# Kernel optimization log

Hardware: AMD Instinct MI355X
Metric: run time of the kernel (lower is better)

The kernel has to match this reference:

```python
import jax, jax.numpy as jnp
import numpy as np

B, C, D = 16, 512, 256
K = 16        # spatio_topk
RD = 128      # rec_dim
H = 8         # num_heads
FFN = 1024    # temporal_ffn
TEMP = 0.5    # temperature


def setup_inputs() -> dict:
    key = jax.random.key(0)
    ks = jax.random.split(key, 8)
    s = lambda k, shape: (jax.random.normal(k, shape, jnp.float32) * 0.02)
    return dict(
        x=jax.random.normal(ks[0], (B, C, D), jnp.float32),
        wq_rec=s(ks[1], (RD, D)),
        wk_rec=s(ks[2], (RD, D)),
        in_proj_w=s(ks[3], (3 * D, D)),
        in_proj_b=jnp.zeros((3 * D,), jnp.float32),
        out_w=s(ks[4], (D, D)),
        out_b=jnp.zeros((D,), jnp.float32),
        ln1_g=jnp.ones((D,), jnp.float32),
        ln1_b=jnp.zeros((D,), jnp.float32),
        mlp_w1=s(ks[5], (FFN, D)),
        mlp_b1=jnp.zeros((FFN,), jnp.float32),
        mlp_w2=s(ks[6], (D, FFN)),
        mlp_b2=jnp.zeros((D,), jnp.float32),
        ln2_g=jnp.ones((D,), jnp.float32),
        ln2_b=jnp.zeros((D,), jnp.float32),
    )


def _ln(x, g, b, eps=1e-5):
    m = x.mean(-1, keepdims=True)
    v = ((x - m) ** 2).mean(-1, keepdims=True)
    return (x - m) * jax.lax.rsqrt(v + eps) * g + b


def reference(x, wq_rec, wk_rec, in_proj_w, in_proj_b, out_w, out_b,
              ln1_g, ln1_b, mlp_w1, mlp_b1, mlp_w2, mlp_b2, ln2_g, ln2_b):
    b, c, d = x.shape
    # --- ST_Rec_Module (training branch: straight-through top-k routing) ---
    xq = x @ wq_rec.T                                   # (B,C,RD)
    xk = x @ wk_rec.T
    logits = jnp.einsum('bqd,bkd->bqk', xq, xk) / TEMP  # (B,C,C)
    idx = jax.lax.top_k(logits, K)[1]                   # (B,C,K)
    z_hard = jax.nn.one_hot(idx, c, dtype=x.dtype)      # (B,C,K,C)
    # cumulative mask of previously-selected channels (exclusive cumsum)
    prev = jnp.cumsum(z_hard, axis=2)
    prev = jnp.concatenate([jnp.zeros_like(prev[:, :, :1]), prev[:, :, :-1]], axis=2)
    mask = prev > 0
    zs = jnp.where(mask, -1e30, logits[:, :, None, :] / TEMP)  # logits/temp twice, as in source
    z_soft = jax.nn.softmax(zs, axis=-1)
    z = z_hard + z_soft - jax.lax.stop_gradient(z_soft)        # straight-through
    rec_x = jnp.einsum('bqkc,bcd->bqkd', z, x)                 # (B,C,K,D)

    # --- ST_Channel_Module: per-channel cross-attention, query length 1 ---
    hd = d // H
    wq, wk, wv = in_proj_w[:d], in_proj_w[d:2 * d], in_proj_w[2 * d:]
    bq, bk, bv = in_proj_b[:d], in_proj_b[d:2 * d], in_proj_b[2 * d:]
    q = (x @ wq.T + bq).reshape(b, c, H, hd)                   # (B,C,H,hd)
    k = (rec_x @ wk.T + bk).reshape(b, c, K, H, hd)
    v = (rec_x @ wv.T + bv).reshape(b, c, K, H, hd)
    scores = jnp.einsum('bchd,bckhd->bchk', q, k) / np.float32(np.sqrt(hd))
    attn = jax.nn.softmax(scores, axis=-1)
    ctx = jnp.einsum('bchk,bckhd->bchd', attn, v).reshape(b, c, d)
    attn_out = ctx @ out_w.T + out_b
    x1 = _ln(attn_out + x, ln1_g, ln1_b)

    # --- ST_Temporal_Module (Identity projections, gelu FFN + LN) ---
    h = jax.nn.gelu(x1 @ mlp_w1.T + mlp_b1, approximate=False)
    h = h @ mlp_w2.T + mlp_b2
    x2 = _ln(h + x1, ln2_g, ln2_b)
    return x2
```

## Files before the change

### kernel.cpp

```cpp
#include <hip/hip_runtime.h>
#include <hip/hip_bf16.h>
#include <math.h>

#define B_   16
#define C_   512
#define D_   256
#define K_   16
#define RD_  128
#define H_   8
#define HD_  32
#define FFN_ 1024
#define M_   (B_ * C_)

typedef __attribute__((ext_vector_type(8))) short bf16x8;
typedef __attribute__((ext_vector_type(4))) float f32x4;

typedef __attribute__((address_space(1))) const int ga_int;
typedef __attribute__((address_space(3))) int ls_int;

static __device__ __forceinline__ short f2bf(float v) {
    __hip_bfloat16 h = __float2bfloat16(v);
    return *(short*)&h;
}
static __device__ __forceinline__ float bf2f(short s) {
    __hip_bfloat16 h = *(__hip_bfloat16*)&s;
    return __bfloat162float(h);
}
static __device__ __forceinline__ float4 ld4bf(const short* p) {
    uint2 u = *(const uint2*)p;
    float4 r;
    r.x = __uint_as_float((u.x & 0xffffu) << 16);
    r.y = __uint_as_float(u.x & 0xffff0000u);
    r.z = __uint_as_float((u.y & 0xffffu) << 16);
    r.w = __uint_as_float(u.y & 0xffff0000u);
    return r;
}

#define N8_X    (M_ * D_ / 8)
#define N8_INW  (768 * D_ / 8)
#define N8_OUTW (D_ * D_ / 8)
#define N8_W1   (FFN_ * D_ / 8)
#define N8_W2   (D_ * FFN_ / 8)
#define N8_WQ   (RD_ * D_ / 8)
#define N8_ALL  (N8_X + N8_INW + N8_OUTW + N8_W1 + N8_W2 + 2 * N8_WQ)

__global__ __launch_bounds__(256) void convert_all_kernel(
    const float* __restrict__ x, const float* __restrict__ inw,
    const float* __restrict__ outw, const float* __restrict__ w1,
    const float* __restrict__ w2, const float* __restrict__ wq,
    const float* __restrict__ wk,
    short* __restrict__ xbf, short* __restrict__ xlo,
    short* __restrict__ inwbf, short* __restrict__ outwbf,
    short* __restrict__ w1bf, short* __restrict__ w2bf,
    short* __restrict__ wqh, short* __restrict__ wql,
    short* __restrict__ wkh, short* __restrict__ wkl)
{
    int i = blockIdx.x * 256 + threadIdx.x;
    if (i >= N8_ALL) return;

    const float* s; short* dh; short* dl = nullptr; int off;
    if      (i < N8_X)                    { s = x;    dh = xbf;    dl = xlo; off = i; }
    else if (i < N8_X + N8_INW)           { s = inw;  dh = inwbf;  off = i - N8_X; }
    else if (i < N8_X + N8_INW + N8_OUTW) { s = outw; dh = outwbf; off = i - N8_X - N8_INW; }
    else if (i < N8_X + N8_INW + N8_OUTW + N8_W1)
                                          { s = w1;   dh = w1bf;   off = i - N8_X - N8_INW - N8_OUTW; }
    else if (i < N8_X + N8_INW + N8_OUTW + N8_W1 + N8_W2)
                                          { s = w2;   dh = w2bf;   off = i - N8_X - N8_INW - N8_OUTW - N8_W1; }
    else if (i < N8_X + N8_INW + N8_OUTW + N8_W1 + N8_W2 + N8_WQ)
                                          { s = wq;   dh = wqh; dl = wql; off = i - N8_X - N8_INW - N8_OUTW - N8_W1 - N8_W2; }
    else                                  { s = wk;   dh = wkh; dl = wkl; off = i - N8_X - N8_INW - N8_OUTW - N8_W1 - N8_W2 - N8_WQ; }

    const float4* sp = (const float4*)s + (size_t)off * 2;
    float4 v0 = sp[0], v1 = sp[1];
    float f[8] = {v0.x, v0.y, v0.z, v0.w, v1.x, v1.y, v1.z, v1.w};
    short rh[8], rl[8];
    #pragma unroll
    for (int j = 0; j < 8; ++j) {
        rh[j] = f2bf(f[j]);
        rl[j] = f2bf(f[j] - bf2f(rh[j]));
    }
    *(bf16x8*)(dh + (size_t)off * 8) = *(bf16x8*)rh;
    if (dl) *(bf16x8*)(dl + (size_t)off * 8) = *(bf16x8*)rl;
}

template<int BM, int BN, int OUT_BF16, int ACT>
__global__ __launch_bounds__(256) void gemm_mfma(
    const short* __restrict__ A, const short* __restrict__ W,
    const float* __restrict__ bias, void* __restrict__ Cout,
    int M, int N, int Kd)
{
    __shared__ short As[2][BM * 32];
    __shared__ short Bs[2][BN * 32];
    const int tid  = threadIdx.x;
    const int wave = tid >> 6;
    const int lane = tid & 63;
    const int bm = blockIdx.y * BM;
    const int bn = blockIdx.x * BN;
    constexpr int MI = BM / 32;
    constexpr int NJ = BN / 32;
    const int wr = (wave >> 1) * (BM / 2);
    const int wc = (wave & 1) * (BN / 2);

    const int fr = lane & 15;
    const int fk = (lane >> 4) * 8;
    const int r0 = tid >> 2, ch = (tid & 3) * 8;

    f32x4 acc[MI][NJ];
    #pragma unroll
    for (int i = 0; i < MI; ++i)
        #pragma unroll
        for (int j = 0; j < NJ; ++j)
            acc[i][j] = (f32x4){0.f, 0.f, 0.f, 0.f};

    auto stage = [&](int buf, int k0) {
        #pragma unroll
        for (int i = 0; i < BM / 64; ++i)
            __builtin_amdgcn_global_load_lds(
                (ga_int*)&A[(size_t)(bm + r0 + i * 64) * Kd + k0 + ch],
                (ls_int*)&As[buf][(tid + i * 256) * 8], 16, 0, 0);
        #pragma unroll
        for (int j = 0; j < BN / 64; ++j)
            __builtin_amdgcn_global_load_lds(
                (ga_int*)&W[(size_t)(bn + r0 + j * 64) * Kd + k0 + ch],
                (ls_int*)&Bs[buf][(tid + j * 256) * 8], 16, 0, 0);
    };

    stage(0, 0);
    int cur = 0;

    for (int k0 = 0; k0 < Kd; k0 += 32) {
        __syncthreads();
        if (k0 + 32 < Kd) stage(cur ^ 1, k0 + 32);

        bf16x8 af[MI], bfr[NJ];
        #pragma unroll
        for (int i = 0; i < MI; ++i) af[i]  = *(bf16x8*)&As[cur][(wr + i * 16 + fr) * 32 + fk];
        #pragma unroll
        for (int j = 0; j < NJ; ++j) bfr[j] = *(bf16x8*)&Bs[cur][(wc + j * 16 + fr) * 32 + fk];
        #pragma unroll
        for (int i = 0; i < MI; ++i)
            #pragma unroll
            for (int j = 0; j < NJ; ++j)
                acc[i][j] = __builtin_amdgcn_mfma_f32_16x16x32_bf16(af[i], bfr[j], acc[i][j], 0, 0, 0);
        cur ^= 1;
    }

    const int rowbase = (lane >> 4) * 4;
    #pragma unroll
    for (int i = 0; i < MI; ++i) {
        #pragma unroll
        for (int j = 0; j < NJ; ++j) {
            const int n = bn + wc + j * 16 + fr;
            const float bn_v = bias ? bias[n] : 0.f;
            #pragma unroll
            for (int r = 0; r < 4; ++r) {
                const int m = bm + wr + i * 16 + rowbase + r;
                float v = acc[i][j][r] + bn_v;
                if (ACT) v = 0.5f * v * (1.0f + erff(v * 0.70710678118654752f));
                if (OUT_BF16) ((short*)Cout)[(size_t)m * N + n] = f2bf(v);
                else          ((float*)Cout)[(size_t)m * N + n] = v;
            }
        }
    }
}

__global__ __launch_bounds__(256) void proj_kernel(
    const short* __restrict__ xbf, const short* __restrict__ xlo,
    const short* __restrict__ inwbf, const float* __restrict__ in_b,
    const short* __restrict__ wqh, const short* __restrict__ wql,
    const short* __restrict__ wkh, const short* __restrict__ wkl,
    short* __restrict__ qkvbf,
    short* __restrict__ qh, short* __restrict__ ql,
    short* __restrict__ kh, short* __restrict__ kl)
{
    __shared__ short smem[12288];
    const int bid  = blockIdx.x;
    const int tid  = threadIdx.x;
    const int wave = tid >> 6;
    const int lane = tid & 63;
    const int fr = lane & 15;
    const int fk = (lane >> 4) * 8;
    const int r0 = tid >> 2, ch = (tid & 3) * 8;

    if (bid < 768) {
        const int bm = (bid / 6) * 64;
        const int bn = (bid % 6) * 128;
        const int wr = (wave >> 1) * 32;
        const int wc = (wave & 1) * 64;
        short* As = smem;
        short* Bs = smem + 4096;

        f32x4 acc[2][4];
        #pragma unroll
        for (int i = 0; i < 2; ++i)
            #pragma unroll
            for (int j = 0; j < 4; ++j)
                acc[i][j] = (f32x4){0.f, 0.f, 0.f, 0.f};

        auto stage = [&](int buf, int k0) {
            __builtin_amdgcn_global_load_lds(
                (ga_int*)&xbf[(size_t)(bm + r0) * D_ + k0 + ch],
                (ls_int*)&As[buf * 2048 + tid * 8], 16, 0, 0);
            #pragma unroll
            for (int j = 0; j < 2; ++j)
                __builtin_amdgcn_global_load_lds(
                    (ga_int*)&inwbf[(size_t)(bn + r0 + j * 64) * D_ + k0 + ch],
                    (ls_int*)&Bs[buf * 4096 + (tid + j * 256) * 8], 16, 0, 0);
        };

        stage(0, 0);
        int cur = 0;
        for (int k0 = 0; k0 < D_; k0 += 32) {
            __syncthreads();
            if (k0 + 32 < D_) stage(cur ^ 1, k0 + 32);
            bf16x8 af[2], bfr[4];
            #pragma unroll
            for (int i = 0; i < 2; ++i) af[i]  = *(bf16x8*)&As[cur * 2048 + (wr + i * 16 + fr) * 32 + fk];
            #pragma unroll
            for (int j = 0; j < 4; ++j) bfr[j] = *(bf16x8*)&Bs[cur * 4096 + (wc + j * 16 + fr) * 32 + fk];
            #pragma unroll
            for (int i = 0; i < 2; ++i)
                #pragma unroll
                for (int j = 0; j < 4; ++j)
                    acc[i][j] = __builtin_amdgcn_mfma_f32_16x16x32_bf16(af[i], bfr[j], acc[i][j], 0, 0, 0);
            cur ^= 1;
        }

        const int rowbase = (lane >> 4) * 4;
        #pragma unroll
        for (int i = 0; i < 2; ++i)
            #pragma unroll
            for (int j = 0; j < 4; ++j) {
                const int n = bn + wc + j * 16 + fr;
                const float bv = in_b[n];
                #pragma unroll
                for (int r = 0; r < 4; ++r) {
                    const int m = bm + wr + i * 16 + rowbase + r;
                    qkvbf[(size_t)m * 768 + n] = f2bf(acc[i][j][r] + bv);
                }
            }
    } else {
        const int t = bid - 768;
        const int z = t >> 8;
        const int rem = t & 255;
        const int bm = (rem >> 1) * 64;
        const int bn = (rem & 1) * 64;
        const short* Wh = z ? wkh : wqh;
        const short* Wl = z ? wkl : wql;
        short* Oh = z ? kh : qh;
        short* Ol = z ? kl : ql;
        short* Ah = smem;
        short* Al = smem + 2048;
        short* Bh = smem + 4096;
        short* Bl = smem + 6144;

        const int wr = (wave >> 1) * 32;
        const int wc = (wave & 1) * 32;

        f32x4 acc[2][2];
        #pragma unroll
        for (int i = 0; i < 2; ++i)
            #pragma unroll
            for (int j = 0; j < 2; ++j)
                acc[i][j] = (f32x4){0.f, 0.f, 0.f, 0.f};

        for (int k0 = 0; k0 < D_; k0 += 32) {
            __builtin_amdgcn_global_load_lds((ga_int*)&xbf[(size_t)(bm + r0) * D_ + k0 + ch], (ls_int*)&Ah[tid * 8], 16, 0, 0);
            __builtin_amdgcn_global_load_lds((ga_int*)&xlo[(size_t)(bm + r0) * D_ + k0 + ch], (ls_int*)&Al[tid * 8], 16, 0, 0);
            __builtin_amdgcn_global_load_lds((ga_int*)&Wh[(size_t)(bn + r0) * D_ + k0 + ch], (ls_int*)&Bh[tid * 8], 16, 0, 0);
            __builtin_amdgcn_global_load_lds((ga_int*)&Wl[(size_t)(bn + r0) * D_ + k0 + ch], (ls_int*)&Bl[tid * 8], 16, 0, 0);
            __syncthreads();

            bf16x8 ah[2], al[2], bh[2], bl[2];
            #pragma unroll
            for (int i = 0; i < 2; ++i) {
                ah[i] = *(bf16x8*)&Ah[(wr + i * 16 + fr) * 32 + fk];
                al[i] = *(bf16x8*)&Al[(wr + i * 16 + fr) * 32 + fk];
            }
            #pragma unroll
            for (int j = 0; j < 2; ++j) {
                bh[j] = *(bf16x8*)&Bh[(wc + j * 16 + fr) * 32 + fk];
                bl[j] = *(bf16x8*)&Bl[(wc + j * 16 + fr) * 32 + fk];
            }
            #pragma unroll
            for (int i = 0; i < 2; ++i)
                #pragma unroll
                for (int j = 0; j < 2; ++j) {
                    acc[i][j] = __builtin_amdgcn_mfma_f32_16x16x32_bf16(ah[i], bh[j], acc[i][j], 0, 0, 0);
                    acc[i][j] = __builtin_amdgcn_mfma_f32_16x16x32_bf16(ah[i], bl[j], acc[i][j], 0, 0, 0);
                    acc[i][j] = __builtin_amdgcn_mfma_f32_16x16x32_bf16(al[i], bh[j], acc[i][j], 0, 0, 0);
                }
            __syncthreads();
        }

        const int rowbase = (lane >> 4) * 4;
        #pragma unroll
        for (int i = 0; i < 2; ++i)
            #pragma unroll
            for (int j = 0; j < 2; ++j) {
                const int n = bn + wc + j * 16 + fr;
                #pragma unroll
                for (int r = 0; r < 4; ++r) {
                    const int m = bm + wr + i * 16 + rowbase + r;
                    float v = acc[i][j][r];
                    short h = f2bf(v);
                    Oh[(size_t)m * RD_ + n] = h;
                    Ol[(size_t)m * RD_ + n] = f2bf(v - bf2f(h));
                }
            }
    }
}

__global__ __launch_bounds__(256) void logits_mfma(
    const short* __restrict__ qh, const short* __restrict__ ql,
    const short* __restrict__ kh, const short* __restrict__ kl,
    float* __restrict__ out)
{
    __shared__ short Ah[64 * 32], Al[64 * 32], Bh[64 * 32], Bl[64 * 32];
    const int tid  = threadIdx.x;
    const int wave = tid >> 6;
    const int lane = tid & 63;
    const int base = blockIdx.z * C_;
    const int bm = blockIdx.y * 64;
    const int bn = blockIdx.x * 64;
    const int wr = (wave >> 1) * 32;
    const int wc = (wave & 1) * 32;
    const int fr = lane & 15;
    const int fk = (lane >> 4) * 8;
    const int r0 = tid >> 2, ch = (tid & 3) * 8;

    f32x4 acc[2][2];
    #pragma unroll
    for (int i = 0; i < 2; ++i)
        #pragma unroll
        for (int j = 0; j < 2; ++j)
            acc[i][j] = (f32x4){0.f, 0.f, 0.f, 0.f};

    for (int k0 = 0; k0 < RD_; k0 += 32) {
        __builtin_amdgcn_global_load_lds((ga_int*)&qh[(size_t)(base + bm + r0) * RD_ + k0 + ch], (ls_int*)&Ah[tid * 8], 16, 0, 0);
        __builtin_amdgcn_global_load_lds((ga_int*)&ql[(size_t)(base + bm + r0) * RD_ + k0 + ch], (ls_int*)&Al[tid * 8], 16, 0, 0);
        __builtin_amdgcn_global_load_lds((ga_int*)&kh[(size_t)(base + bn + r0) * RD_ + k0 + ch], (ls_int*)&Bh[tid * 8], 16, 0, 0);
        __builtin_amdgcn_global_load_lds((ga_int*)&kl[(size_t)(base + bn + r0) * RD_ + k0 + ch], (ls_int*)&Bl[tid * 8], 16, 0, 0);
        __syncthreads();

        bf16x8 ah[2], al[2], bh[2], bl[2];
        #pragma unroll
        for (int i = 0; i < 2; ++i) {
            ah[i] = *(bf16x8*)&Ah[(wr + i * 16 + fr) * 32 + fk];
            al[i] = *(bf16x8*)&Al[(wr + i * 16 + fr) * 32 + fk];
        }
        #pragma unroll
        for (int j = 0; j < 2; ++j) {
            bh[j] = *(bf16x8*)&Bh[(wc + j * 16 + fr) * 32 + fk];
            bl[j] = *(bf16x8*)&Bl[(wc + j * 16 + fr) * 32 + fk];
        }
        #pragma unroll
        for (int i = 0; i < 2; ++i)
            #pragma unroll
            for (int j = 0; j < 2; ++j) {
                acc[i][j] = __builtin_amdgcn_mfma_f32_16x16x32_bf16(ah[i], bh[j], acc[i][j], 0, 0, 0);
                acc[i][j] = __builtin_amdgcn_mfma_f32_16x16x32_bf16(ah[i], bl[j], acc[i][j], 0, 0, 0);
                acc[i][j] = __builtin_amdgcn_mfma_f32_16x16x32_bf16(al[i], bh[j], acc[i][j], 0, 0, 0);
            }
        __syncthreads();
    }

    const int rowbase = (lane >> 4) * 4;
    #pragma unroll
    for (int i = 0; i < 2; ++i)
        #pragma unroll
        for (int j = 0; j < 2; ++j) {
            const int n = bn + wc + j * 16 + fr;
            #pragma unroll
            for (int r = 0; r < 4; ++r) {
                const int m = base + bm + wr + i * 16 + rowbase + r;
                out[(size_t)m * C_ + n] = acc[i][j][r];
            }
        }
}

__global__ __launch_bounds__(256) void topk_attn_kernel(
    const float* __restrict__ logits, const short* __restrict__ qkv,
    short* __restrict__ ctxbf)
{
    const int wave = threadIdx.x >> 6;
    const int lane = threadIdx.x & 63;
    const int row  = blockIdx.x * 4 + wave;
    const int bbase = row & ~(C_ - 1);

    const float* lrow = logits + (size_t)row * C_;
    float v[8];
    #pragma unroll
    for (int j = 0; j < 8; ++j) v[j] = lrow[lane * 8 + j];

    int ii[K_];
    #pragma unroll
    for (int sel = 0; sel < K_; ++sel) {
        float bv = v[0]; int bj = 0;
        #pragma unroll
        for (int j = 1; j < 8; ++j)
            if (v[j] > bv) { bv = v[j]; bj = j; }
        float wb = bv;
        #pragma unroll
        for (int s = 1; s < 64; s <<= 1)
            wb = fmaxf(wb, __shfl_xor(wb, s, 64));
        unsigned long long mask = __ballot(bv == wb);
        int wl = __ffsll(mask) - 1;
        int wj = __shfl(bj, wl, 64);
        ii[sel] = wl * 8 + wj;
        #pragma unroll
        for (int j = 0; j < 8; ++j)
            if (lane == wl && bj == j) v[j] = -INFINITY;
    }

    const short* qrow = qkv + (size_t)row * 768;
    float4 qv = ld4bf(qrow + lane * 4);

    float s[K_];
    #pragma unroll
    for (int k = 0; k < K_; ++k) {
        float4 kv = ld4bf(qkv + (size_t)(bbase + ii[k]) * 768 + 256 + lane * 4);
        float p = qv.x * kv.x + qv.y * kv.y + qv.z * kv.z + qv.w * kv.w;
        p += __shfl_xor(p, 1, 64);
        p += __shfl_xor(p, 2, 64);
        p += __shfl_xor(p, 4, 64);
        s[k] = p * 0.17677669529663687f;
    }

    float m = s[0];
    #pragma unroll
    for (int k = 1; k < K_; ++k) m = fmaxf(m, s[k]);
    float ssum = 0.f;
    #pragma unroll
    for (int k = 0; k < K_; ++k) { s[k] = __expf(s[k] - m); ssum += s[k]; }
    const float inv = 1.f / ssum;

    float4 acc = {0.f, 0.f, 0.f, 0.f};
    #pragma unroll
    for (int k = 0; k < K_; ++k) {
        float4 vvv = ld4bf(qkv + (size_t)(bbase + ii[k]) * 768 + 512 + lane * 4);
        float w = s[k] * inv;
        acc.x += w * vvv.x; acc.y += w * vvv.y; acc.z += w * vvv.z; acc.w += w * vvv.w;
    }

    unsigned lo = (unsigned)(unsigned short)f2bf(acc.x) | ((unsigned)(unsigned short)f2bf(acc.y) << 16);
    unsigned hi = (unsigned)(unsigned short)f2bf(acc.z) | ((unsigned)(unsigned short)f2bf(acc.w) << 16);
    uint2 pk = {lo, hi};
    *(uint2*)(ctxbf + (size_t)row * D_ + lane * 4) = pk;
}

template<int KD, int WBF>
__global__ __launch_bounds__(256) void gemm_ln_mfma(
    const short* __restrict__ A, const short* __restrict__ W,
    const float* __restrict__ bias, const float* __restrict__ res,
    const float* __restrict__ g, const float* __restrict__ beta,
    float* __restrict__ out, short* __restrict__ outbf)
{
    __shared__ short As[2][16 * 32];
    __shared__ short Bs[2][256 * 32];
    __shared__ float part[4][16][2];

    const int tid  = threadIdx.x;
    const int wave = tid >> 6;
    const int lane = tid & 63;
    const int bm = blockIdx.x * 16;
    const int wc = wave * 64;
    const int fr = lane & 15;
    const int fk = (lane >> 4) * 8;
    const int r0 = tid >> 2, ch = (tid & 3) * 8;

    f32x4 acc[4];
    #pragma unroll
    for (int j = 0; j < 4; ++j) acc[j] = (f32x4){0.f, 0.f, 0.f, 0.f};

    auto stage = [&](int buf, int k0) {
        if (tid < 64)
            __builtin_amdgcn_global_load_lds(
                (ga_int*)&A[(size_t)(bm + r0) * KD + k0 + ch],
                (ls_int*)&As[buf][tid * 8], 16, 0, 0);
        #pragma unroll
        for (int j = 0; j < 4; ++j)
            __builtin_amdgcn_global_load_lds(
                (ga_int*)&W[(size_t)(r0 + j * 64) * KD + k0 + ch],
                (ls_int*)&Bs[buf][(tid + j * 256) * 8], 16, 0, 0);
    };

    stage(0, 0);
    int cur = 0;

    for (int k0 = 0; k0 < KD; k0 += 32) {
        __syncthreads();
        if (k0 + 32 < KD) stage(cur ^ 1, k0 + 32);

        bf16x8 af = *(bf16x8*)&As[cur][fr * 32 + fk];
        bf16x8 bfr[4];
        #pragma unroll
        for (int j = 0; j < 4; ++j) bfr[j] = *(bf16x8*)&Bs[cur][(wc + j * 16 + fr) * 32 + fk];
        #pragma unroll
        for (int j = 0; j < 4; ++j)
            acc[j] = __builtin_amdgcn_mfma_f32_16x16x32_bf16(af, bfr[j], acc[j], 0, 0, 0);
        cur ^= 1;
    }

    const int rowbase = (lane >> 4) * 4;
    float vv[4][4];
    float sum[4] = {0.f, 0.f, 0.f, 0.f};
    float sq[4]  = {0.f, 0.f, 0.f, 0.f};

    #pragma unroll
    for (int j = 0; j < 4; ++j) {
        const int n = wc + j * 16 + fr;
        const float bv = bias[n];
        #pragma unroll
        for (int r = 0; r < 4; ++r) {
            const int m = bm + rowbase + r;
            float v = acc[j][r] + bv + res[(size_t)m * D_ + n];
            vv[j][r] = v;
            sum[r] += v;
            sq[r]  += v * v;
        }
    }

    #pragma unroll
    for (int r = 0; r < 4; ++r)
        #pragma unroll
        for (int s = 1; s < 16; s <<= 1) {
            sum[r] += __shfl_xor(sum[r], s, 64);
            sq[r]  += __shfl_xor(sq[r],  s, 64);
        }

    if (fr == 0) {
        #pragma unroll
        for (int r = 0; r < 4; ++r) {
            part[wave][rowbase + r][0] = sum[r];
            part[wave][rowbase + r][1] = sq[r];
        }
    }
    __syncthreads();

    #pragma unroll
    for (int r = 0; r < 4; ++r) {
        const int ml = rowbase + r;
        const float S = part[0][ml][0] + part[1][ml][0] + part[2][ml][0] + part[3][ml][0];
        const float Q = part[0][ml][1] + part[1][ml][1] + part[2][ml][1] + part[3][ml][1];
        const float mean = S * (1.0f / D_);
        const float var  = Q * (1.0f / D_) - mean * mean;
        const float rstd = rsqrtf(var + 1e-5f);
        const int m = bm + ml;
        #pragma unroll
        for (int j = 0; j < 4; ++j) {
            const int n = wc + j * 16 + fr;
            float o = (vv[j][r] - mean) * rstd * g[n] + beta[n];
            out[(size_t)m * D_ + n] = o;
            if (WBF) outbf[(size_t)m * D_ + n] = f2bf(o);
        }
    }
}

extern "C" void kernel_launch(void* const* d_in, const int* in_sizes, int n_in,
                              void* d_out, int out_size, void* d_ws, size_t ws_size,
                              hipStream_t stream)
{
    const float* x      = (const float*)d_in[0];
    const float* wq_rec = (const float*)d_in[1];
    const float* wk_rec = (const float*)d_in[2];
    const float* in_w   = (const float*)d_in[3];
    const float* in_b   = (const float*)d_in[4];
    const float* out_w  = (const float*)d_in[5];
    const float* out_b  = (const float*)d_in[6];
    const float* ln1_g  = (const float*)d_in[7];
    const float* ln1_b  = (const float*)d_in[8];
    const float* w1     = (const float*)d_in[9];
    const float* b1     = (const float*)d_in[10];
    const float* w2     = (const float*)d_in[11];
    const float* b2     = (const float*)d_in[12];
    const float* ln2_g  = (const float*)d_in[13];
    const float* ln2_b  = (const float*)d_in[14];
    float* out = (float*)d_out;

    short* qkvbf = (short*)d_ws;
    short* qh    = qkvbf + (size_t)M_ * 768;
    short* ql    = qh + (size_t)M_ * RD_;
    short* kh    = ql + (size_t)M_ * RD_;
    short* kl    = kh + (size_t)M_ * RD_;
    float* x1    = (float*)(kl + (size_t)M_ * RD_);
    float* U     = x1 + (size_t)M_ * D_;
    float* logits = U;
    short* ctxbf  = (short*)(U + (size_t)M_ * 512);
    short* x1bf   = ctxbf + (size_t)M_ * D_;
    short* hbf    = x1bf  + (size_t)M_ * D_;
    short* xbf    = hbf   + (size_t)M_ * FFN_;
    short* xlo    = xbf   + (size_t)M_ * D_;
    short* inwbf  = xlo   + (size_t)M_ * D_;
    short* outwbf = inwbf + (size_t)768 * D_;
    short* w1bf   = outwbf + (size_t)D_ * D_;
    short* w2bf   = w1bf  + (size_t)FFN_ * D_;
    short* wqh    = w2bf  + (size_t)D_ * FFN_;
    short* wql    = wqh + (size_t)RD_ * D_;
    short* wkh    = wql + (size_t)RD_ * D_;
    short* wkl    = wkh + (size_t)RD_ * D_;

    dim3 blk(256);

    convert_all_kernel<<<dim3((N8_ALL + 255) / 256), blk, 0, stream>>>(
        x, in_w, out_w, w1, w2, wq_rec, wk_rec,
        xbf, xlo, inwbf, outwbf, w1bf, w2bf, wqh, wql, wkh, wkl);

    proj_kernel<<<dim3(1280), blk, 0, stream>>>(
        xbf, xlo, inwbf, in_b, wqh, wql, wkh, wkl, qkvbf, qh, ql, kh, kl);
    logits_mfma<<<dim3(C_ / 64, C_ / 64, B_), blk, 0, stream>>>(qh, ql, kh, kl, logits);
    topk_attn_kernel<<<dim3(M_ / 4), blk, 0, stream>>>(logits, qkvbf, ctxbf);
    gemm_ln_mfma<256, 1><<<dim3(M_ / 16), blk, 0, stream>>>(
        ctxbf, outwbf, out_b, x, ln1_g, ln1_b, x1, x1bf);
    gemm_mfma<64, 128, 1, 1><<<dim3(FFN_ / 128, M_ / 64), blk, 0, stream>>>(x1bf, w1bf, b1, hbf, M_, FFN_, D_);
    gemm_ln_mfma<1024, 0><<<dim3(M_ / 16), blk, 0, stream>>>(
        hbf, w2bf, b2, x1, ln2_g, ln2_b, out, nullptr);
}
```

Before: 106.3 us.

## Fuse top-k attention with output projection and LayerNorm into one kernel

Merges the top-k routing/attention kernel with the out-projection GEMM + residual + LayerNorm kernel. Each block computes the ctx rows for its 16 rows in LDS, then runs the MFMA GEMM against the out weights while prefetching weight tiles, and ends with the LayerNorm epilogue. This removes the global write and re-read of the bf16 ctx buffer and one kernel launch. In exchange, each block now does four rows of top-k serially per wave before the GEMM, which lowers parallelism and may leave the GEMM phase with less latency hiding.

New measurement: 111.7 us. 1.05x slower.

```diff
diff --git a/kernel.cpp b/kernel.cpp
--- a/kernel.cpp
+++ b/kernel.cpp
@@ -379,74 +379,173 @@
         }
 }
 
-__global__ __launch_bounds__(256) void topk_attn_kernel(
+__global__ __launch_bounds__(256) void attn_ln_kernel(
     const float* __restrict__ logits, const short* __restrict__ qkv,
-    short* __restrict__ ctxbf)
+    const short* __restrict__ W, const float* __restrict__ bias,
+    const float* __restrict__ res, const float* __restrict__ g,
+    const float* __restrict__ beta,
+    float* __restrict__ out, short* __restrict__ outbf)
 {
-    const int wave = threadIdx.x >> 6;
-    const int lane = threadIdx.x & 63;
-    const int row  = blockIdx.x * 4 + wave;
-    const int bbase = row & ~(C_ - 1);
-
-    const float* lrow = logits + (size_t)row * C_;
-    float v[8];
-    #pragma unroll
-    for (int j = 0; j < 8; ++j) v[j] = lrow[lane * 8 + j];
-
-    int ii[K_];
-    #pragma unroll
-    for (int sel = 0; sel < K_; ++sel) {
-        float bv = v[0]; int bj = 0;
-        #pragma unroll
-        for (int j = 1; j < 8; ++j)
-            if (v[j] > bv) { bv = v[j]; bj = j; }
-        float wb = bv;
-        #pragma unroll
-        for (int s = 1; s < 64; s <<= 1)
-            wb = fmaxf(wb, __shfl_xor(wb, s, 64));
-        unsigned long long mask = __ballot(bv == wb);
-        int wl = __ffsll(mask) - 1;
-        int wj = __shfl(bj, wl, 64);
-        ii[sel] = wl * 8 + wj;
-        #pragma unroll
-        for (int j = 0; j < 8; ++j)
-            if (lane == wl && bj == j) v[j] = -INFINITY;
-    }
-
-    const short* qrow = qkv + (size_t)row * 768;
-    float4 qv = ld4bf(qrow + lane * 4);
-
-    float s[K_];
-    #pragma unroll
-    for (int k = 0; k < K_; ++k) {
-        float4 kv = ld4bf(qkv + (size_t)(bbase + ii[k]) * 768 + 256 + lane * 4);
-        float p = qv.x * kv.x + qv.y * kv.y + qv.z * kv.z + qv.w * kv.w;
-        p += __shfl_xor(p, 1, 64);
-        p += __shfl_xor(p, 2, 64);
-        p += __shfl_xor(p, 4, 64);
-        s[k] = p * 0.17677669529663687f;
-    }
-
-    float m = s[0];
-    #pragma unroll
-    for (int k = 1; k < K_; ++k) m = fmaxf(m, s[k]);
-    float ssum = 0.f;
-    #pragma unroll
-    for (int k = 0; k < K_; ++k) { s[k] = __expf(s[k] - m); ssum += s[k]; }
-    const float inv = 1.f / ssum;
-
-    float4 acc = {0.f, 0.f, 0.f, 0.f};
-    #pragma unroll
-    for (int k = 0; k < K_; ++k) {
-        float4 vvv = ld4bf(qkv + (size_t)(bbase + ii[k]) * 768 + 512 + lane * 4);
-        float w = s[k] * inv;
-        acc.x += w * vvv.x; acc.y += w * vvv.y; acc.z += w * vvv.z; acc.w += w * vvv.w;
-    }
-
-    unsigned lo = (unsigned)(unsigned short)f2bf(acc.x) | ((unsigned)(unsigned short)f2bf(acc.y) << 16);
-    unsigned hi = (unsigned)(unsigned short)f2bf(acc.z) | ((unsigned)(unsigned short)f2bf(acc.w) << 16);
-    uint2 pk = {lo, hi};
-    *(uint2*)(ctxbf + (size_t)row * D_ + lane * 4) = pk;
+    __shared__ short ctxlds[16 * 256];
+    __shared__ short Bs[2][256 * 32];
+    __shared__ float part[4][16][2];
+
+    const int tid  = threadIdx.x;
+    const int wave = tid >> 6;
+    const int lane = tid & 63;
+    const int bm = blockIdx.x * 16;
+    const int wc = wave * 64;
+    const int fr = lane & 15;
+    const int fk = (lane >> 4) * 8;
+    const int r0 = tid >> 2, ch = (tid & 3) * 8;
+
+    auto stageB = [&](int buf, int k0) {
+        #pragma unroll
+        for (int j = 0; j < 4; ++j)
+            __builtin_amdgcn_global_load_lds(
+                (ga_int*)&W[(size_t)(r0 + j * 64) * D_ + k0 + ch],
+                (ls_int*)&Bs[buf][(tid + j * 256) * 8], 16, 0, 0);
+    };
+
+    stageB(0, 0);
+
+    for (int rq = 0; rq < 4; ++rq) {
+        const int lrow_i = bm + wave * 4 + rq;
+        const int bbase = lrow_i & ~(C_ - 1);
+        const float* lrow = logits + (size_t)lrow_i * C_;
+
+        float v[8];
+        #pragma unroll
+        for (int j = 0; j < 8; ++j) v[j] = lrow[lane * 8 + j];
+
+        int ii[K_];
+        #pragma unroll
+        for (int sel = 0; sel < K_; ++sel) {
+            float bv = v[0]; int bj = 0;
+            #pragma unroll
+            for (int j = 1; j < 8; ++j)
+                if (v[j] > bv) { bv = v[j]; bj = j; }
+            float wb = bv;
+            #pragma unroll
+            for (int s = 1; s < 64; s <<= 1)
+                wb = fmaxf(wb, __shfl_xor(wb, s, 64));
+            unsigned long long mask = __ballot(bv == wb);
+            int wl = __ffsll(mask) - 1;
+            int wj = __shfl(bj, wl, 64);
+            ii[sel] = wl * 8 + wj;
+            #pragma unroll
+            for (int j = 0; j < 8; ++j)
+                if (lane == wl && bj == j) v[j] = -INFINITY;
+        }
+
+        float4 qv = ld4bf(qkv + (size_t)lrow_i * 768 + lane * 4);
+
+        float s[K_];
+        #pragma unroll
+        for (int k = 0; k < K_; ++k) {
+            float4 kv = ld4bf(qkv + (size_t)(bbase + ii[k]) * 768 + 256 + lane * 4);
+            float p = qv.x * kv.x + qv.y * kv.y + qv.z * kv.z + qv.w * kv.w;
+            p += __shfl_xor(p, 1, 64);
+            p += __shfl_xor(p, 2, 64);
+            p += __shfl_xor(p, 4, 64);
+            s[k] = p * 0.17677669529663687f;
+        }
+
+        float m = s[0];
+        #pragma unroll
+        for (int k = 1; k < K_; ++k) m = fmaxf(m, s[k]);
+        float ssum = 0.f;
+        #pragma unroll
+        for (int k = 0; k < K_; ++k) { s[k] = __expf(s[k] - m); ssum += s[k]; }
+        const float inv = 1.f / ssum;
+
+        float4 acc4 = {0.f, 0.f, 0.f, 0.f};
+        #pragma unroll
+        for (int k = 0; k < K_; ++k) {
+            float4 vvv = ld4bf(qkv + (size_t)(bbase + ii[k]) * 768 + 512 + lane * 4);
+            float w = s[k] * inv;
+            acc4.x += w * vvv.x; acc4.y += w * vvv.y; acc4.z += w * vvv.z; acc4.w += w * vvv.w;
+        }
+
+        unsigned lo = (unsigned)(unsigned short)f2bf(acc4.x) | ((unsigned)(unsigned short)f2bf(acc4.y) << 16);
+        unsigned hi = (unsigned)(unsigned short)f2bf(acc4.z) | ((unsigned)(unsigned short)f2bf(acc4.w) << 16);
+        uint2 pk = {lo, hi};
+        const int c0 = lane * 4;
+        *(uint2*)&ctxlds[(c0 >> 5) * 512 + (wave * 4 + rq) * 32 + (c0 & 31)] = pk;
+    }
+
+    f32x4 acc[4];
+    #pragma unroll
+    for (int j = 0; j < 4; ++j) acc[j] = (f32x4){0.f, 0.f, 0.f, 0.f};
+
+    int cur = 0;
+    for (int k0 = 0; k0 < D_; k0 += 32) {
+        __syncthreads();
+        if (k0 + 32 < D_) stageB(cur ^ 1, k0 + 32);
+
+        bf16x8 af = *(bf16x8*)&ctxlds[(k0 >> 5) * 512 + fr * 32 + fk];
+        bf16x8 bfr[4];
+        #pragma unroll
+        for (int j = 0; j < 4; ++j) bfr[j] = *(bf16x8*)&Bs[cur][(wc + j * 16 + fr) * 32 + fk];
+        #pragma unroll
+        for (int j = 0; j < 4; ++j)
+            acc[j] = __builtin_amdgcn_mfma_f32_16x16x32_bf16(af, bfr[j], acc[j], 0, 0, 0);
+        cur ^= 1;
+    }
+
+    const int rowbase = (lane >> 4) * 4;
+    float vv[4][4];
+    float sum[4] = {0.f, 0.f, 0.f, 0.f};
+    float sq[4]  = {0.f, 0.f, 0.f, 0.f};
+
+    #pragma unroll
+    for (int j = 0; j < 4; ++j) {
+        const int n = wc + j * 16 + fr;
+        const float bv = bias[n];
+        #pragma unroll
+        for (int r = 0; r < 4; ++r) {
+            const int m = bm + rowbase + r;
+            float v = acc[j][r] + bv + res[(size_t)m * D_ + n];
+            vv[j][r] = v;
+            sum[r] += v;
+            sq[r]  += v * v;
+        }
+    }
+
+    #pragma unroll
+    for (int r = 0; r < 4; ++r)
+        #pragma unroll
+        for (int s = 1; s < 16; s <<= 1) {
+            sum[r] += __shfl_xor(sum[r], s, 64);
+            sq[r]  += __shfl_xor(sq[r],  s, 64);
+        }
+
+    if (fr == 0) {
+        #pragma unroll
+        for (int r = 0; r < 4; ++r) {
+            part[wave][rowbase + r][0] = sum[r];
+            part[wave][rowbase + r][1] = sq[r];
+        }
+    }
+    __syncthreads();
+
+    #pragma unroll
+    for (int r = 0; r < 4; ++r) {
+        const int ml = rowbase + r;
+        const float S = part[0][ml][0] + part[1][ml][0] + part[2][ml][0] + part[3][ml][0];
+        const float Q = part[0][ml][1] + part[1][ml][1] + part[2][ml][1] + part[3][ml][1];
+        const float mean = S * (1.0f / D_);
+        const float var  = Q * (1.0f / D_) - mean * mean;
+        const float rstd = rsqrtf(var + 1e-5f);
+        const int m = bm + ml;
+        #pragma unroll
+        for (int j = 0; j < 4; ++j) {
+            const int n = wc + j * 16 + fr;
+            float o = (vv[j][r] - mean) * rstd * g[n] + beta[n];
+            out[(size_t)m * D_ + n] = o;
+            outbf[(size_t)m * D_ + n] = f2bf(o);
+        }
+    }
 }
 
 template<int KD, int WBF>
@@ -586,8 +685,7 @@
     float* x1    = (float*)(kl + (size_t)M_ * RD_);
     float* U     = x1 + (size_t)M_ * D_;
     float* logits = U;
-    short* ctxbf  = (short*)(U + (size_t)M_ * 512);
-    short* x1bf   = ctxbf + (size_t)M_ * D_;
+    short* x1bf   = (short*)(U + (size_t)M_ * 512);
     short* hbf    = x1bf  + (size_t)M_ * D_;
     short* xbf    = hbf   + (size_t)M_ * FFN_;
     short* xlo    = xbf   + (size_t)M_ * D_;
@@ -609,9 +707,8 @@
     proj_kernel<<<dim3(1280), blk, 0, stream>>>(
         xbf, xlo, inwbf, in_b, wqh, wql, wkh, wkl, qkvbf, qh, ql, kh, kl);
     logits_mfma<<<dim3(C_ / 64, C_ / 64, B_), blk, 0, stream>>>(qh, ql, kh, kl, logits);
-    topk_attn_kernel<<<dim3(M_ / 4), blk, 0, stream>>>(logits, qkvbf, ctxbf);
-    gemm_ln_mfma<256, 1><<<dim3(M_ / 16), blk, 0, stream>>>(
-        ctxbf, outwbf, out_b, x, ln1_g, ln1_b, x1, x1bf);
+    attn_ln_kernel<<<dim3(M_ / 16), blk, 0, stream>>>(
+        logits, qkvbf, outwbf, out_b, x, ln1_g, ln1_b, x1, x1bf);
     gemm_mfma<64, 128, 1, 1><<<dim3(FFN_ / 128, M_ / 64), blk, 0, stream>>>(x1bf, w1bf, b1, hbf, M_, FFN_, D_);
     gemm_ln_mfma<1024, 0><<<dim3(M_ / 16), blk, 0, stream>>>(
         hbf, w2bf, b2, x1, ln2_g, ln2_b, out, nullptr);
```
